# Kernel optimization log

Hardware: AMD Instinct MI355X
Metric: run time of the kernel (lower is better)

## Reference

```python
import jax, jax.numpy as jnp
import numpy as np

N = 1048576      # number of samples
D = 128          # feature dim
NUM_CLASS = 100  # number of anchor classes


def setup_inputs() -> dict:
    key = jax.random.key(0)
    kx, ka, ky = jax.random.split(key, 3)
    x = jax.random.normal(kx, (N, D), dtype=jnp.float32)
    anchors = jax.random.normal(ka, (NUM_CLASS, D), dtype=jnp.float32)
    y = jax.random.randint(ky, (N,), 0, NUM_CLASS, dtype=jnp.int64)
    return {"x": x, "anchors": anchors, "y": y}


def reference(x, anchors, y):
    # scores of every sample against every class anchor: [N, C]
    scores = jnp.einsum('nd,cd->nc', x, anchors)
    # original computes -log(exp(s_y) / sum_c exp(s_c)) per sample == cross-entropy;
    # log_softmax is the numerically stable equivalent of the same math.
    logp = jax.nn.log_softmax(scores, axis=-1)
    ce = -jnp.take_along_axis(logp, y[:, None].astype(jnp.int32), axis=1)[:, 0]  # [N]
    mean_ce = jnp.mean(ce)
    # the outer python loop over unique labels (reject_threshold=0) adds mean CE
    # once per label that appears at least once in y
    counts = jax.ops.segment_sum(jnp.ones_like(y, dtype=jnp.int32), y.astype(jnp.int32),
                                 num_segments=NUM_CLASS)
    n_present = jnp.sum(counts > 0).astype(mean_ce.dtype)
    return mean_ce * n_present
```

## Files before the change

### kernel.cpp

```cpp
#include <hip/hip_runtime.h>
#include <hip/hip_bf16.h>

#define DFEAT 128
#define NCLASS 100
#define NTPAD 7

typedef short bf16x8 __attribute__((ext_vector_type(8)));
typedef float f32x4  __attribute__((ext_vector_type(4)));

__device__ __forceinline__ short f2bf(float f) {
    unsigned u = __float_as_uint(f);
    u += 0x7fffu + ((u >> 16) & 1u);
    return (short)(u >> 16);
}

__device__ __forceinline__ bf16x8 cvt8_rne(float4 f0, float4 f1) {
    bf16x8 v;
    v[0] = f2bf(f0.x); v[1] = f2bf(f0.y); v[2] = f2bf(f0.z); v[3] = f2bf(f0.w);
    v[4] = f2bf(f1.x); v[5] = f2bf(f1.y); v[6] = f2bf(f1.z); v[7] = f2bf(f1.w);
    return v;
}

__device__ __forceinline__ bf16x8 cvt8_trunc(float4 f0, float4 f1) {
    union { bf16x8 v; unsigned u[4]; } r;
    r.u[0] = __builtin_amdgcn_perm(__float_as_uint(f0.y), __float_as_uint(f0.x), 0x07060302u);
    r.u[1] = __builtin_amdgcn_perm(__float_as_uint(f0.w), __float_as_uint(f0.z), 0x07060302u);
    r.u[2] = __builtin_amdgcn_perm(__float_as_uint(f1.y), __float_as_uint(f1.x), 0x07060302u);
    r.u[3] = __builtin_amdgcn_perm(__float_as_uint(f1.w), __float_as_uint(f1.z), 0x07060302u);
    return r.v;
}

__global__ __launch_bounds__(256, 2)
void ce_main(const float* __restrict__ x, const float* __restrict__ anchors,
             const int* __restrict__ y, int ntiles,
             float* __restrict__ total_ce, unsigned* __restrict__ gpres) {
    __shared__ unsigned spres[4];
    if (threadIdx.x < 4) spres[threadIdx.x] = 0u;
    __syncthreads();

    const int lane = threadIdx.x & 63;
    const int c    = lane & 15;
    const int q    = lane >> 4;
    const int wid    = blockIdx.x * 4 + (threadIdx.x >> 6);
    const int nwaves = gridDim.x * 4;

    bf16x8 bf[NTPAD][4];
    #pragma unroll
    for (int t = 0; t < NTPAD; ++t) {
        const int col = t * 16 + c;
        #pragma unroll
        for (int kk = 0; kk < 4; ++kk) {
            if (col < NCLASS) {
                const float4* av = (const float4*)anchors + (size_t)col * (DFEAT / 4) + q * 2 + kk * 8;
                bf[t][kk] = cvt8_rne(av[0], av[1]);
            } else {
                bf16x8 z = {0,0,0,0,0,0,0,0};
                bf[t][kk] = z;
            }
        }
    }

    float acc_ce = 0.f;

    float4 cur[8];
    int    curY = 0;
    int tile = wid;
    if (tile < ntiles) {
        const float4* xv = (const float4*)x + (size_t)(tile * 16 + c) * (DFEAT / 4) + q * 2;
        #pragma unroll
        for (int kk = 0; kk < 4; ++kk) { cur[2 * kk] = xv[kk * 8]; cur[2 * kk + 1] = xv[kk * 8 + 1]; }
        curY = y[tile * 16 + c];
    }

    for (; tile < ntiles; tile += nwaves) {
        bf16x8 af[4];
        #pragma unroll
        for (int kk = 0; kk < 4; ++kk) af[kk] = cvt8_trunc(cur[2 * kk], cur[2 * kk + 1]);
        const int Yl = curY;

        const int nxt = tile + nwaves;
        if (nxt < ntiles) {
            const float4* xv = (const float4*)x + (size_t)(nxt * 16 + c) * (DFEAT / 4) + q * 2;
            #pragma unroll
            for (int kk = 0; kk < 4; ++kk) { cur[2 * kk] = xv[kk * 8]; cur[2 * kk + 1] = xv[kk * 8 + 1]; }
            curY = y[nxt * 16 + c];
        }

        if (q == 0) atomicOr(&spres[Yl >> 5], 1u << (Yl & 31));

        f32x4 acc[NTPAD];
        #pragma unroll
        for (int t = 0; t < NTPAD; ++t) { f32x4 z = {0.f, 0.f, 0.f, 0.f}; acc[t] = z; }
        #pragma unroll
        for (int kk = 0; kk < 4; ++kk)
            #pragma unroll
            for (int t = 0; t < NTPAD; ++t)
                acc[t] = __builtin_amdgcn_mfma_f32_16x16x32_bf16(af[kk], bf[t][kk], acc[t], 0, 0, 0);

        #pragma unroll
        for (int r = 0; r < 4; ++r) {
            const int Yr = __shfl(Yl, q * 4 + r, 64);
            float l = 0.f, sy = 0.f;
            #pragma unroll
            for (int t = 0; t < NTPAD; ++t) {
                const int col = t * 16 + c;
                const float s = acc[t][r];
                l += __expf(s);
                if (col == Yr) sy = s;
            }
            l += __shfl_xor(l, 1, 64);  sy += __shfl_xor(sy, 1, 64);
            l += __shfl_xor(l, 2, 64);  sy += __shfl_xor(sy, 2, 64);
            l += __shfl_xor(l, 4, 64);  sy += __shfl_xor(sy, 4, 64);
            l += __shfl_xor(l, 8, 64);  sy += __shfl_xor(sy, 8, 64);

            if (c == 0) acc_ce += __logf(l - 12.0f) - sy;
        }
    }

    acc_ce += __shfl_xor(acc_ce, 1, 64);
    acc_ce += __shfl_xor(acc_ce, 2, 64);
    acc_ce += __shfl_xor(acc_ce, 4, 64);
    acc_ce += __shfl_xor(acc_ce, 8, 64);
    acc_ce += __shfl_xor(acc_ce, 16, 64);
    acc_ce += __shfl_xor(acc_ce, 32, 64);
    if (lane == 0) atomicAdd(total_ce, acc_ce);

    __syncthreads();
    if (threadIdx.x < 4) atomicOr(&gpres[threadIdx.x], spres[threadIdx.x]);
}

__global__ void ce_finalize(const float* __restrict__ total_ce,
                            const unsigned* __restrict__ pres,
                            float* __restrict__ out, int nsamples) {
    if (threadIdx.x == 0 && blockIdx.x == 0) {
        int np = 0;
        #pragma unroll
        for (int i = 0; i < 4; ++i) np += __popc(pres[i]);
        out[0] = total_ce[0] * ((float)np / (float)nsamples);
    }
}

extern "C" void kernel_launch(void* const* d_in, const int* in_sizes, int n_in,
                              void* d_out, int out_size, void* d_ws, size_t ws_size,
                              hipStream_t stream) {
    const float* x       = (const float*)d_in[0];
    const float* anchors = (const float*)d_in[1];
    const int*   y       = (const int*)d_in[2];
    float* out = (float*)d_out;

    const int nsamples = in_sizes[0] / DFEAT;
    const int ntiles   = nsamples / 16;

    float*    total = (float*)d_ws;
    unsigned* pres  = (unsigned*)((char*)d_ws + 16);

    hipMemsetAsync(d_ws, 0, 64, stream);
    ce_main<<<512, 256, 0, stream>>>(x, anchors, y, ntiles, total, pres);
    ce_finalize<<<1, 64, 0, stream>>>(total, pres, out, nsamples);
}
```

Measured before the change: 715.7 us.

## Transpose MFMA operands so each lane reduces its classes locally, use exp2

Swaps the MFMA A/B operands so each lane's accumulator holds four classes for one sample. Most of the softmax sum then happens in registers and needs only two cross-lane shuffles, replacing four per-row shuffle trees plus a label broadcast. log2(e) is folded into the bf16 anchors so exp2/log2 can be used, with a ln2 rescale in finalize. Label-presence tracking moves from per-tile LDS atomics to register bitmasks that are OR-reduced once per wave. The main cost targeted is the shuffle- and transcendental-heavy epilogue, at the price of slightly different rounding from scaling anchors before the bf16 conversion.

```diff
diff --git a/kernel.cpp b/kernel.cpp
--- a/kernel.cpp
+++ b/kernel.cpp
@@ -14,10 +14,10 @@
     return (short)(u >> 16);
 }
 
-__device__ __forceinline__ bf16x8 cvt8_rne(float4 f0, float4 f1) {
+__device__ __forceinline__ bf16x8 cvt8_rne_scaled(float4 f0, float4 f1, float sc) {
     bf16x8 v;
-    v[0] = f2bf(f0.x); v[1] = f2bf(f0.y); v[2] = f2bf(f0.z); v[3] = f2bf(f0.w);
-    v[4] = f2bf(f1.x); v[5] = f2bf(f1.y); v[6] = f2bf(f1.z); v[7] = f2bf(f1.w);
+    v[0] = f2bf(f0.x * sc); v[1] = f2bf(f0.y * sc); v[2] = f2bf(f0.z * sc); v[3] = f2bf(f0.w * sc);
+    v[4] = f2bf(f1.x * sc); v[5] = f2bf(f1.y * sc); v[6] = f2bf(f1.z * sc); v[7] = f2bf(f1.w * sc);
     return v;
 }
 
@@ -34,16 +34,13 @@
 void ce_main(const float* __restrict__ x, const float* __restrict__ anchors,
              const int* __restrict__ y, int ntiles,
              float* __restrict__ total_ce, unsigned* __restrict__ gpres) {
-    __shared__ unsigned spres[4];
-    if (threadIdx.x < 4) spres[threadIdx.x] = 0u;
-    __syncthreads();
-
     const int lane = threadIdx.x & 63;
     const int c    = lane & 15;
     const int q    = lane >> 4;
     const int wid    = blockIdx.x * 4 + (threadIdx.x >> 6);
     const int nwaves = gridDim.x * 4;
 
+    const float LOG2E = 1.4426950408889634f;
     bf16x8 bf[NTPAD][4];
     #pragma unroll
     for (int t = 0; t < NTPAD; ++t) {
@@ -52,7 +49,7 @@
         for (int kk = 0; kk < 4; ++kk) {
             if (col < NCLASS) {
                 const float4* av = (const float4*)anchors + (size_t)col * (DFEAT / 4) + q * 2 + kk * 8;
-                bf[t][kk] = cvt8_rne(av[0], av[1]);
+                bf[t][kk] = cvt8_rne_scaled(av[0], av[1], LOG2E);
             } else {
                 bf16x8 z = {0,0,0,0,0,0,0,0};
                 bf[t][kk] = z;
@@ -61,6 +58,7 @@
     }
 
     float acc_ce = 0.f;
+    unsigned pm0 = 0, pm1 = 0, pm2 = 0, pm3 = 0;
 
     float4 cur[8];
     int    curY = 0;
@@ -86,7 +84,14 @@
             curY = y[nxt * 16 + c];
         }
 
-        if (q == 0) atomicOr(&spres[Yl >> 5], 1u << (Yl & 31));
+        {
+            const int w = Yl >> 5;
+            const unsigned b = 1u << (Yl & 31);
+            pm0 |= (w == 0) ? b : 0u;
+            pm1 |= (w == 1) ? b : 0u;
+            pm2 |= (w == 2) ? b : 0u;
+            pm3 |= (w == 3) ? b : 0u;
+        }
 
         f32x4 acc[NTPAD];
         #pragma unroll
@@ -95,26 +100,25 @@
         for (int kk = 0; kk < 4; ++kk)
             #pragma unroll
             for (int t = 0; t < NTPAD; ++t)
-                acc[t] = __builtin_amdgcn_mfma_f32_16x16x32_bf16(af[kk], bf[t][kk], acc[t], 0, 0, 0);
+                acc[t] = __builtin_amdgcn_mfma_f32_16x16x32_bf16(bf[t][kk], af[kk], acc[t], 0, 0, 0);
 
+        const int yq = Yl - (q << 2);
+        float lp[4] = {0.f, 0.f, 0.f, 0.f};
+        float syn = 0.f;
         #pragma unroll
-        for (int r = 0; r < 4; ++r) {
-            const int Yr = __shfl(Yl, q * 4 + r, 64);
-            float l = 0.f, sy = 0.f;
+        for (int t = 0; t < NTPAD; ++t) {
             #pragma unroll
-            for (int t = 0; t < NTPAD; ++t) {
-                const int col = t * 16 + c;
+            for (int r = 0; r < 4; ++r) {
                 const float s = acc[t][r];
-                l += __expf(s);
-                if (col == Yr) sy = s;
+                lp[r] += exp2f(s);
+                if (yq == t * 16 + r) syn = s;
             }
-            l += __shfl_xor(l, 1, 64);  sy += __shfl_xor(sy, 1, 64);
-            l += __shfl_xor(l, 2, 64);  sy += __shfl_xor(sy, 2, 64);
-            l += __shfl_xor(l, 4, 64);  sy += __shfl_xor(sy, 4, 64);
-            l += __shfl_xor(l, 8, 64);  sy += __shfl_xor(sy, 8, 64);
-
-            if (c == 0) acc_ce += __logf(l - 12.0f) - sy;
         }
+        float l = (lp[0] + lp[1]) + (lp[2] + lp[3]);
+        l += __shfl_xor(l, 16, 64);
+        l += __shfl_xor(l, 32, 64);
+        acc_ce -= syn;
+        if (q == 0) acc_ce += __log2f(l - 12.0f);
     }
 
     acc_ce += __shfl_xor(acc_ce, 1, 64);
@@ -125,8 +129,19 @@
     acc_ce += __shfl_xor(acc_ce, 32, 64);
     if (lane == 0) atomicAdd(total_ce, acc_ce);
 
-    __syncthreads();
-    if (threadIdx.x < 4) atomicOr(&gpres[threadIdx.x], spres[threadIdx.x]);
+    #pragma unroll
+    for (int s = 1; s <= 32; s <<= 1) {
+        pm0 |= (unsigned)__shfl_xor((int)pm0, s, 64);
+        pm1 |= (unsigned)__shfl_xor((int)pm1, s, 64);
+        pm2 |= (unsigned)__shfl_xor((int)pm2, s, 64);
+        pm3 |= (unsigned)__shfl_xor((int)pm3, s, 64);
+    }
+    if (lane == 0) {
+        atomicOr(&gpres[0], pm0);
+        atomicOr(&gpres[1], pm1);
+        atomicOr(&gpres[2], pm2);
+        atomicOr(&gpres[3], pm3);
+    }
 }
 
 __global__ void ce_finalize(const float* __restrict__ total_ce,
@@ -136,7 +151,7 @@
         int np = 0;
         #pragma unroll
         for (int i = 0; i < 4; ++i) np += __popc(pres[i]);
-        out[0] = total_ce[0] * ((float)np / (float)nsamples);
+        out[0] = total_ce[0] * 0.69314718055994530942f * ((float)np / (float)nsamples);
     }
 }
 
```

New measurement: 797.4 us. +11.4%, slower.
